# Performance work log

Measured on AMD Instinct MI355X. Metric: run time of the kernel, lower is better.

## Reference

```python
import jax, jax.numpy as jnp
import numpy as np

N_NODES = 50000
N_EDGES = 1600000
IN_NF, IN_EF, H1, H2, OUT_NF = 64, 16, 32, 32, 64
MH1, MH2, MH3 = 64, 128, 64


def _linear_params(key, fan_in, fan_out):
    kw, kb = jax.random.split(key)
    s = 1.0 / np.sqrt(fan_in)
    W = jax.random.uniform(kw, (fan_in, fan_out), minval=-s, maxval=s, dtype=jnp.float32)
    b = jax.random.uniform(kb, (fan_out,), minval=-s, maxval=s, dtype=jnp.float32)
    return W, b


def setup_inputs() -> dict:
    key = jax.random.key(0)
    ks = jax.random.split(key, 12)
    nf = jax.random.normal(ks[0], (N_NODES, IN_NF), dtype=jnp.float32)
    ef = jax.random.normal(ks[1], (N_EDGES, IN_EF), dtype=jnp.float32)
    src = jax.random.randint(ks[2], (N_EDGES,), 0, N_NODES)
    dst = jax.random.randint(ks[3], (N_EDGES,), 0, N_NODES)
    # MLP_msg: (2*in_nf+in_ef) -> 64 -> 128 -> 64 -> (1+h1+h2)
    Wm1, bm1 = _linear_params(ks[4], 2 * IN_NF + IN_EF, MH1)
    Wm2, bm2 = _linear_params(ks[5], MH1, MH2)
    Wm3, bm3 = _linear_params(ks[6], MH2, MH3)
    Wm4, bm4 = _linear_params(ks[7], MH3, 1 + H1 + H2)
    # MLP_reduce: (in_nf+h1+h2) -> 64 -> 128 -> 64 -> out_nf
    Wr1, br1 = _linear_params(ks[8], IN_NF + H1 + H2, MH1)
    Wr2, br2 = _linear_params(ks[9], MH1, MH2)
    Wr3, br3 = _linear_params(ks[10], MH2, MH3)
    Wr4, br4 = _linear_params(ks[11], MH3, OUT_NF)
    return {"nf": nf, "ef": ef, "src": src, "dst": dst,
            "Wm1": Wm1, "bm1": bm1, "Wm2": Wm2, "bm2": bm2,
            "Wm3": Wm3, "bm3": bm3, "Wm4": Wm4, "bm4": bm4,
            "Wr1": Wr1, "br1": br1, "Wr2": Wr2, "br2": br2,
            "Wr3": Wr3, "br3": br3, "Wr4": Wr4, "br4": br4}


def _mlp(x, Ws, bs):
    n = len(Ws)
    for i, (W, b) in enumerate(zip(Ws, bs)):
        x = x @ W + b
        if i < n - 1:
            x = jax.nn.leaky_relu(x, negative_slope=0.2)
    return x


def reference(nf, ef, src, dst,
              Wm1, bm1, Wm2, bm2, Wm3, bm3, Wm4, bm4,
              Wr1, br1, Wr2, br2, Wr3, br3, Wr4, br4):
    # edge_udf: gather src/dst node feats + edge feats, per-edge MLP, sigmoid gate
    x = jnp.concatenate([nf[src], nf[dst], ef], axis=1)  # [E, 2*in_nf+in_ef]
    x = _mlp(x, [Wm1, Wm2, Wm3, Wm4], [bm1, bm2, bm3, bm4])  # [E, 1+h1+h2]
    k = jax.nn.sigmoid(x[:, :1])
    ef1 = x[:, 1:1 + H1] * k
    ef2 = x[:, 1 + H1:] * k
    # update_all: scatter-sum of ef1, scatter-max of ef2 onto destination nodes
    nf1 = jax.ops.segment_sum(ef1, dst, num_segments=N_NODES)
    nf2 = jax.ops.segment_max(ef2, dst, num_segments=N_NODES)
    nf2 = jnp.where(jnp.isfinite(nf2), nf2, 0.0)  # DGL fills 0 for nodes with no in-edges
    y = jnp.concatenate([nf, nf1, nf2], axis=1)  # [N, in_nf+h1+h2]
    return _mlp(y, [Wr1, Wr2, Wr3, Wr4], [br1, br2, br3, br4])
```

## Files before the change

kernel.cpp:

```cpp
#include <hip/hip_runtime.h>

typedef unsigned int u32;
typedef __attribute__((ext_vector_type(8))) short short8;
typedef __attribute__((ext_vector_type(4))) short short4v;
typedef __attribute__((ext_vector_type(4))) float f32x4;

__device__ __forceinline__ float lrelu(float x){ return x > 0.f ? x : 0.2f*x; }

__device__ __forceinline__ void atomicMaxF(float* a, float v){
  if (__float_as_int(v) >= 0) atomicMax((int*)a, __float_as_int(v));
  else                        atomicMin((u32*)a, __float_as_uint(v));
}

__global__ void init_ws(float* __restrict__ nf1, float* __restrict__ nf2, int n32){
  int i = blockIdx.x*blockDim.x + threadIdx.x;
  int st = gridDim.x*blockDim.x;
  for (; i < n32; i += st){ nf1[i] = 0.f; nf2[i] = -__builtin_inff(); }
}

struct HL { short hi, lo; };
__device__ __forceinline__ HL split1(float x){
  u32 u = __float_as_uint(x);
  u32 r = u + 0x7FFFu + ((u >> 16) & 1u);
  float l = x - __uint_as_float(r & 0xFFFF0000u);
  HL o; o.hi = (short)(r >> 16); o.lo = (short)(__float_as_uint(l) >> 16);
  return o;
}

__device__ __forceinline__ void gatherB(const float* __restrict__ W, int K, int Nout,
                                        int kbase, int n, short8& hi, short8& lo){
  #pragma unroll
  for (int j = 0; j < 8; ++j){
    int k = kbase + j;
    float w = (k < K && n < Nout) ? W[(size_t)k * Nout + n] : 0.f;
    HL s = split1(w); hi[j] = s.hi; lo[j] = s.lo;
  }
}

__device__ __forceinline__ f32x4 mfma3(short8 ah, short8 al, short8 bh, short8 bl, f32x4 c){
  c = __builtin_amdgcn_mfma_f32_16x16x32_bf16(ah, bh, c, 0, 0, 0);
  c = __builtin_amdgcn_mfma_f32_16x16x32_bf16(al, bh, c, 0, 0, 0);
  c = __builtin_amdgcn_mfma_f32_16x16x32_bf16(ah, bl, c, 0, 0, 0);
  return c;
}

__device__ __forceinline__ void sstore1(short* hp, short* lp, int idx, float x){
  HL s = split1(x); hp[idx] = s.hi; lp[idx] = s.lo;
}
__device__ __forceinline__ void sstore4(short* hp, short* lp, int idx, f32x4 v){
  short4v h, l;
  #pragma unroll
  for (int j = 0; j < 4; ++j){ HL s = split1(v[j]); h[j] = s.hi; l[j] = s.lo; }
  *(short4v*)(hp + idx) = h;
  *(short4v*)(lp + idx) = l;
}

__global__ __launch_bounds__(256, 2) void node_pre(
    const float* __restrict__ nf, const float* __restrict__ Wm1,
    float* __restrict__ P, int N)
{
  __shared__ short Xnh[32*72];
  __shared__ short Xnl[32*72];

  const int lane = threadIdx.x & 63, wv = threadIdx.x >> 6;
  const int nl = lane & 15, quad = lane >> 4;
  const int nb = wv;
  const int slot = wv*4 + quad;

  short8 Bah[2], Bal[2], Bbh[2], Bbl[2];
  #pragma unroll
  for (int kc = 0; kc < 2; ++kc){
    gatherB(Wm1, 144, 64, kc*32 + quad*8,      nb*16 + nl, Bah[kc], Bal[kc]);
    gatherB(Wm1, 144, 64, 64 + kc*32 + quad*8, nb*16 + nl, Bbh[kc], Bbl[kc]);
  }

  const int ntiles = (N + 31) >> 5;
  for (int t = blockIdx.x; t < ntiles; t += gridDim.x){
    const int base = t << 5;
    #pragma unroll
    for (int r2 = 0; r2 < 2; ++r2){
      int row = slot*2 + r2;
      int n = base + row;
      int nc = n < N ? n : 0;
      f32x4 v = *(const f32x4*)(nf + (size_t)nc*64 + nl*4);
      sstore4(Xnh, Xnl, row*72 + nl*4, v);
    }
    __syncthreads();

    f32x4 aa[2] = {{0,0,0,0},{0,0,0,0}};
    f32x4 ab[2] = {{0,0,0,0},{0,0,0,0}};
    #pragma unroll
    for (int kc = 0; kc < 2; ++kc)
      #pragma unroll
      for (int mb = 0; mb < 2; ++mb){
        int ro = (mb*16 + nl)*72 + kc*32 + quad*8;
        short8 ah = *(const short8*)(Xnh + ro);
        short8 al = *(const short8*)(Xnl + ro);
        aa[mb] = mfma3(ah, al, Bah[kc], Bal[kc], aa[mb]);
        ab[mb] = mfma3(ah, al, Bbh[kc], Bbl[kc], ab[mb]);
      }
    #pragma unroll
    for (int mb = 0; mb < 2; ++mb)
      #pragma unroll
      for (int r = 0; r < 4; ++r){
        int n = base + mb*16 + quad*4 + r;
        if (n < N){
          P[(size_t)n*128 +      nb*16 + nl] = aa[mb][r];
          P[(size_t)n*128 + 64 + nb*16 + nl] = ab[mb][r];
        }
      }
    __syncthreads();
  }
}

#define PXES  40
#define PSS   68
#define PH1S  72
#define PH2S  136
#define POFF_XEL  1280
#define POFF_S    2560
#define POFF_H1H  6912
#define POFF_H1L  9216
#define POFF_H2H  11520
#define POFF_H2L  15872
#define POFF_DST  20224
#define P_LDS_SHORTS 20352
#define P_LDS_BYTES  (P_LDS_SHORTS*2)

__global__ __launch_bounds__(256, 2) void edge_mfma_p(
    const float* __restrict__ P, const float* __restrict__ ef,
    const int* __restrict__ src, const int* __restrict__ dst,
    const float* __restrict__ Wm1, const float* __restrict__ bm1,
    const float* __restrict__ Wm2, const float* __restrict__ bm2,
    const float* __restrict__ Wm3, const float* __restrict__ bm3,
    const float* __restrict__ Wm4, const float* __restrict__ bm4,
    float* __restrict__ nf1, float* __restrict__ nf2, int E)
{
  extern __shared__ short smem[];
  short* Xeh = smem;
  short* Xel = smem + POFF_XEL;
  float* Sb  = (float*)(smem + POFF_S);
  short* H1h = smem + POFF_H1H;
  short* H1l = smem + POFF_H1L;
  short* H2h = smem + POFF_H2H;
  short* H2l = smem + POFF_H2L;
  int*  dstI = (int*)(smem + POFF_DST);

  {
    float* z = (float*)smem;
    for (int i = threadIdx.x; i < POFF_XEL; i += blockDim.x) z[i] = 0.f;
  }

  const int lane = threadIdx.x & 63, wv = threadIdx.x >> 6;
  const int nl = lane & 15, quad = lane >> 4;
  const int nb1 = wv;
  const int slot = wv*4 + quad;

  short8 B1ch, B1cl;
  gatherB(Wm1, 144, 64, 128 + quad*8, nb1*16 + nl, B1ch, B1cl);
  short8 B2h[2][2], B2l[2][2];
  #pragma unroll
  for (int i = 0; i < 2; ++i)
    #pragma unroll
    for (int kc = 0; kc < 2; ++kc) gatherB(Wm2, 64, 128, kc*32 + quad*8, (nb1 + i*4)*16 + nl, B2h[i][kc], B2l[i][kc]);
  short8 B3h[4], B3l[4];
  #pragma unroll
  for (int kc = 0; kc < 4; ++kc) gatherB(Wm3, 128, 64,  kc*32 + quad*8, nb1*16 + nl, B3h[kc], B3l[kc]);
  short8 B4h[2], B4l[2];
  #pragma unroll
  for (int kc = 0; kc < 2; ++kc) gatherB(Wm4, 64, 65, kc*32 + quad*8, nb1*16 + nl, B4h[kc], B4l[kc]);
  const int gcol = (nl < 8) ? 0 : 64;
  short8 Bgh[2], Bgl[2];
  #pragma unroll
  for (int kc = 0; kc < 2; ++kc) gatherB(Wm4, 64, 65, kc*32 + quad*8, gcol, Bgh[kc], Bgl[kc]);

  const float bi1  = bm1[nb1*16 + nl];
  const float bi2a = bm2[nb1*16 + nl], bi2b = bm2[(nb1+4)*16 + nl];
  const float bi3  = bm3[nb1*16 + nl];
  const float bi4a = bm4[nb1*16 + nl];
  const float big  = bm4[gcol];
  __syncthreads();

  const int ntiles = (E + 31) >> 5;
  int pp = 0;
  for (int t = blockIdx.x; t < ntiles; t += gridDim.x, pp ^= 1){
    #pragma unroll
    for (int r2 = 0; r2 < 2; ++r2){
      int row = slot*2 + r2;
      int e = (t << 5) + row;
      int ec = e < E ? e : 0;
      int s = src[ec], d = dst[ec];
      f32x4 a = *(const f32x4*)(P + (size_t)s*128 +      nl*4);
      f32x4 b = *(const f32x4*)(P + (size_t)d*128 + 64 + nl*4);
      f32x4 sv = a + b;
      *(f32x4*)(Sb + row*PSS + nl*4) = sv;
      if (nl < 4){
        f32x4 v2 = *(const f32x4*)(ef + (size_t)ec*16 + nl*4);
        sstore4(Xeh, Xel, row*PXES + nl*4, v2);
      }
      if (nl == 5) dstI[pp*32 + row] = (e < E) ? d : -1;
    }
    __syncthreads();

    {
      f32x4 a1[2] = {{bi1,bi1,bi1,bi1},{bi1,bi1,bi1,bi1}};
      #pragma unroll
      for (int mb = 0; mb < 2; ++mb){
        int ro = (mb*16 + nl)*PXES + quad*8;
        short8 ah = *(const short8*)(Xeh + ro);
        short8 al = *(const short8*)(Xel + ro);
        a1[mb] = mfma3(ah, al, B1ch, B1cl, a1[mb]);
      }
      #pragma unroll
      for (int mb = 0; mb < 2; ++mb)
        #pragma unroll
        for (int r = 0; r < 4; ++r){
          int row = mb*16 + quad*4 + r;
          float sv = Sb[row*PSS + nb1*16 + nl];
          sstore1(H1h, H1l, row*PH1S + nb1*16 + nl, lrelu(a1[mb][r] + sv));
        }
    }
    __syncthreads();

    {
      f32x4 a2a[2] = {{bi2a,bi2a,bi2a,bi2a},{bi2a,bi2a,bi2a,bi2a}};
      f32x4 a2b[2] = {{bi2b,bi2b,bi2b,bi2b},{bi2b,bi2b,bi2b,bi2b}};
      #pragma unroll
      for (int kc = 0; kc < 2; ++kc)
        #pragma unroll
        for (int mb = 0; mb < 2; ++mb){
          int ro = (mb*16 + nl)*PH1S + kc*32 + quad*8;
          short8 ah = *(const short8*)(H1h + ro);
          short8 al = *(const short8*)(H1l + ro);
          a2a[mb] = mfma3(ah, al, B2h[0][kc], B2l[0][kc], a2a[mb]);
          a2b[mb] = mfma3(ah, al, B2h[1][kc], B2l[1][kc], a2b[mb]);
        }
      #pragma unroll
      for (int mb = 0; mb < 2; ++mb)
        #pragma unroll
        for (int r = 0; r < 4; ++r){
          int row = mb*16 + quad*4 + r;
          sstore1(H2h, H2l, row*PH2S + nb1*16 + nl,     lrelu(a2a[mb][r]));
          sstore1(H2h, H2l, row*PH2S + (nb1+4)*16 + nl, lrelu(a2b[mb][r]));
        }
    }
    __syncthreads();

    {
      f32x4 a3[2] = {{bi3,bi3,bi3,bi3},{bi3,bi3,bi3,bi3}};
      #pragma unroll
      for (int kc = 0; kc < 4; ++kc)
        #pragma unroll
        for (int mb = 0; mb < 2; ++mb){
          int ro = (mb*16 + nl)*PH2S + kc*32 + quad*8;
          short8 ah = *(const short8*)(H2h + ro);
          short8 al = *(const short8*)(H2l + ro);
          a3[mb] = mfma3(ah, al, B3h[kc], B3l[kc], a3[mb]);
        }
      #pragma unroll
      for (int mb = 0; mb < 2; ++mb)
        #pragma unroll
        for (int r = 0; r < 4; ++r)
          sstore1(H1h, H1l, (mb*16 + quad*4 + r)*PH1S + nb1*16 + nl, lrelu(a3[mb][r]));
    }
    __syncthreads();

    {
      f32x4 a4[2] = {{bi4a,bi4a,bi4a,bi4a},{bi4a,bi4a,bi4a,bi4a}};
      f32x4 ag[2] = {{big,big,big,big},{big,big,big,big}};
      #pragma unroll
      for (int kc = 0; kc < 2; ++kc)
        #pragma unroll
        for (int mb = 0; mb < 2; ++mb){
          int ro = (mb*16 + nl)*PH1S + kc*32 + quad*8;
          short8 ah = *(const short8*)(H1h + ro);
          short8 al = *(const short8*)(H1l + ro);
          a4[mb] = mfma3(ah, al, B4h[kc], B4l[kc], a4[mb]);
          ag[mb] = mfma3(ah, al, Bgh[kc], Bgl[kc], ag[mb]);
        }
      const int n = nb1*16 + nl;
      #pragma unroll
      for (int mb = 0; mb < 2; ++mb)
        #pragma unroll
        for (int r = 0; r < 4; ++r){
          int row = mb*16 + quad*4 + r;
          float glog = __shfl(ag[mb][r], lane & 0x30);
          float g = 1.f/(1.f + __expf(-glog));
          int d = dstI[pp*32 + row];
          if (d >= 0){
            float v = a4[mb][r] * g;
            if (n >= 1 && n <= 32)  atomicAdd(nf1 + (size_t)d*32 + (n-1), v);
            else if (n >= 33)       atomicMaxF(nf2 + (size_t)d*32 + (n-33), v);
            if (nb1 == 0 && nl == 8)
              atomicMaxF(nf2 + (size_t)d*32 + 31, ag[mb][r] * g);
          }
        }
    }
  }
}

#define XS   168
#define H1S  72
#define H2S  136
#define OFF_XL   5376
#define OFF_H2H  0
#define OFF_H2L  4352
#define OFF_H1H  10752
#define OFF_H1L  13056
#define OFF_DST  15360
#define LDS_SHORTS 15488
#define LDS_BYTES  (LDS_SHORTS*2)

__global__ __launch_bounds__(256, 2) void edge_mfma(
    const float* __restrict__ nf, const float* __restrict__ ef,
    const int* __restrict__ src, const int* __restrict__ dst,
    const float* __restrict__ Wm1, const float* __restrict__ bm1,
    const float* __restrict__ Wm2, const float* __restrict__ bm2,
    const float* __restrict__ Wm3, const float* __restrict__ bm3,
    const float* __restrict__ Wm4, const float* __restrict__ bm4,
    float* __restrict__ nf1, float* __restrict__ nf2, int E)
{
  extern __shared__ short smem[];
  short* Xh  = smem;
  short* Xl  = smem + OFF_XL;
  short* H2h = smem + OFF_H2H;
  short* H2l = smem + OFF_H2L;
  short* H1h = smem + OFF_H1H;
  short* H1l = smem + OFF_H1L;
  int*  dstI = (int*)(smem + OFF_DST);

  const int lane = threadIdx.x & 63, wv = threadIdx.x >> 6;
  const int nl = lane & 15, quad = lane >> 4;
  const int nb1 = wv;
  const int slot = wv*4 + quad;

  short8 B1h[5], B1l[5];
  #pragma unroll
  for (int kc = 0; kc < 5; ++kc) gatherB(Wm1, 144, 64,  kc*32 + quad*8, nb1*16 + nl, B1h[kc], B1l[kc]);
  short8 B2h[2][2], B2l[2][2];
  #pragma unroll
  for (int i = 0; i < 2; ++i)
    #pragma unroll
    for (int kc = 0; kc < 2; ++kc) gatherB(Wm2, 64, 128, kc*32 + quad*8, (nb1 + i*4)*16 + nl, B2h[i][kc], B2l[i][kc]);
  short8 B3h[4], B3l[4];
  #pragma unroll
  for (int kc = 0; kc < 4; ++kc) gatherB(Wm3, 128, 64,  kc*32 + quad*8, nb1*16 + nl, B3h[kc], B3l[kc]);
  short8 B4h[2], B4l[2];
  #pragma unroll
  for (int kc = 0; kc < 2; ++kc) gatherB(Wm4, 64, 65, kc*32 + quad*8, nb1*16 + nl, B4h[kc], B4l[kc]);
  const int gcol = (nl < 8) ? 0 : 64;
  short8 Bgh[2], Bgl[2];
  #pragma unroll
  for (int kc = 0; kc < 2; ++kc) gatherB(Wm4, 64, 65, kc*32 + quad*8, gcol, Bgh[kc], Bgl[kc]);

  const float bi1  = bm1[nb1*16 + nl];
  const float bi2a = bm2[nb1*16 + nl], bi2b = bm2[(nb1+4)*16 + nl];
  const float bi3  = bm3[nb1*16 + nl];
  const float bi4a = bm4[nb1*16 + nl];
  const float big  = bm4[gcol];

  const int ntiles = (E + 31) >> 5;
  int pp = 0;
  for (int t = blockIdx.x; t < ntiles; t += gridDim.x, pp ^= 1){
    #pragma unroll
    for (int r2 = 0; r2 < 2; ++r2){
      int row = slot*2 + r2;
      int e = (t << 5) + row;
      int ec = e < E ? e : 0;
      int s = src[ec], d = dst[ec];
      f32x4 v0 = *(const f32x4*)(nf + (size_t)s*64 + nl*4);
      f32x4 v1 = *(const f32x4*)(nf + (size_t)d*64 + nl*4);
      sstore4(Xh, Xl, row*XS + nl*4,      v0);
      sstore4(Xh, Xl, row*XS + 64 + nl*4, v1);
      if (nl < 4){
        f32x4 v2 = *(const f32x4*)(ef + (size_t)ec*16 + nl*4);
        sstore4(Xh, Xl, row*XS + 128 + nl*4, v2);
      } else if (nl < 8){
        short4v z = {0,0,0,0};
        *(short4v*)(Xh + row*XS + 144 + (nl-4)*4) = z;
        *(short4v*)(Xl + row*XS + 144 + (nl-4)*4) = z;
      }
      if (nl == 5) dstI[pp*32 + row] = (e < E) ? d : -1;
    }
    __syncthreads();

    {
      f32x4 a1[2] = {{bi1,bi1,bi1,bi1},{bi1,bi1,bi1,bi1}};
      #pragma unroll
      for (int kc = 0; kc < 5; ++kc)
        #pragma unroll
        for (int mb = 0; mb < 2; ++mb){
          int ro = (mb*16 + nl)*XS + kc*32 + quad*8;
          short8 ah = *(const short8*)(Xh + ro);
          short8 al = *(const short8*)(Xl + ro);
          a1[mb] = mfma3(ah, al, B1h[kc], B1l[kc], a1[mb]);
        }
      #pragma unroll
      for (int mb = 0; mb < 2; ++mb)
        #pragma unroll
        for (int r = 0; r < 4; ++r)
          sstore1(H1h, H1l, (mb*16 + quad*4 + r)*H1S + nb1*16 + nl, lrelu(a1[mb][r]));
    }
    __syncthreads();

    {
      f32x4 a2a[2] = {{bi2a,bi2a,bi2a,bi2a},{bi2a,bi2a,bi2a,bi2a}};
      f32x4 a2b[2] = {{bi2b,bi2b,bi2b,bi2b},{bi2b,bi2b,bi2b,bi2b}};
      #pragma unroll
      for (int kc = 0; kc < 2; ++kc)
        #pragma unroll
        for (int mb = 0; mb < 2; ++mb){
          int ro = (mb*16 + nl)*H1S + kc*32 + quad*8;
          short8 ah = *(const short8*)(H1h + ro);
          short8 al = *(const short8*)(H1l + ro);
          a2a[mb] = mfma3(ah, al, B2h[0][kc], B2l[0][kc], a2a[mb]);
          a2b[mb] = mfma3(ah, al, B2h[1][kc], B2l[1][kc], a2b[mb]);
        }
      #pragma unroll
      for (int mb = 0; mb < 2; ++mb)
        #pragma unroll
        for (int r = 0; r < 4; ++r){
          int row = mb*16 + quad*4 + r;
          sstore1(H2h, H2l, row*H2S + nb1*16 + nl,     lrelu(a2a[mb][r]));
          sstore1(H2h, H2l, row*H2S + (nb1+4)*16 + nl, lrelu(a2b[mb][r]));
        }
    }
    __syncthreads();

    {
      f32x4 a3[2] = {{bi3,bi3,bi3,bi3},{bi3,bi3,bi3,bi3}};
      #pragma unroll
      for (int kc = 0; kc < 4; ++kc)
        #pragma unroll
        for (int mb = 0; mb < 2; ++mb){
          int ro = (mb*16 + nl)*H2S + kc*32 + quad*8;
          short8 ah = *(const short8*)(H2h + ro);
          short8 al = *(const short8*)(H2l + ro);
          a3[mb] = mfma3(ah, al, B3h[kc], B3l[kc], a3[mb]);
        }
      #pragma unroll
      for (int mb = 0; mb < 2; ++mb)
        #pragma unroll
        for (int r = 0; r < 4; ++r)
          sstore1(H1h, H1l, (mb*16 + quad*4 + r)*H1S + nb1*16 + nl, lrelu(a3[mb][r]));
    }
    __syncthreads();

    {
      f32x4 a4[2] = {{bi4a,bi4a,bi4a,bi4a},{bi4a,bi4a,bi4a,bi4a}};
      f32x4 ag[2] = {{big,big,big,big},{big,big,big,big}};
      #pragma unroll
      for (int kc = 0; kc < 2; ++kc)
        #pragma unroll
        for (int mb = 0; mb < 2; ++mb){
          int ro = (mb*16 + nl)*H1S + kc*32 + quad*8;
          short8 ah = *(const short8*)(H1h + ro);
          short8 al = *(const short8*)(H1l + ro);
          a4[mb] = mfma3(ah, al, B4h[kc], B4l[kc], a4[mb]);
          ag[mb] = mfma3(ah, al, Bgh[kc], Bgl[kc], ag[mb]);
        }
      const int n = nb1*16 + nl;
      #pragma unroll
      for (int mb = 0; mb < 2; ++mb)
        #pragma unroll
        for (int r = 0; r < 4; ++r){
          int row = mb*16 + quad*4 + r;
          float glog = __shfl(ag[mb][r], lane & 0x30);
          float g = 1.f/(1.f + __expf(-glog));
          int d = dstI[pp*32 + row];
          if (d >= 0){
            float v = a4[mb][r] * g;
            if (n >= 1 && n <= 32)  atomicAdd(nf1 + (size_t)d*32 + (n-1), v);
            else if (n >= 33)       atomicMaxF(nf2 + (size_t)d*32 + (n-33), v);
            if (nb1 == 0 && nl == 8)
              atomicMaxF(nf2 + (size_t)d*32 + 31, ag[mb][r] * g);
          }
        }
    }
  }
}

__device__ void zero_f(float* p, int n){
  for (int i = threadIdx.x; i < n; i += blockDim.x) p[i] = 0.f;
}

#define B1S 68
#define C0S 132

__device__ __forceinline__ void splitA(const float* arow, int k0, short8& hi, short8& lo){
  f32x4 x0 = *(const f32x4*)(arow + k0);
  f32x4 x1 = *(const f32x4*)(arow + k0 + 4);
  #pragma unroll
  for (int j = 0; j < 4; ++j){
    HL a = split1(x0[j]); hi[j]   = a.hi; lo[j]   = a.lo;
    HL b = split1(x1[j]); hi[4+j] = b.hi; lo[4+j] = b.lo;
  }
}

__global__ __launch_bounds__(512, 2) void node_mfma(
    const float* __restrict__ nf,
    const float* __restrict__ nf1, const float* __restrict__ nf2,
    const float* __restrict__ Wr1, const float* __restrict__ br1,
    const float* __restrict__ Wr2, const float* __restrict__ br2,
    const float* __restrict__ Wr3, const float* __restrict__ br3,
    const float* __restrict__ Wr4, const float* __restrict__ br4,
    float* __restrict__ out, int N)
{
  __shared__ float buf0[32*C0S];
  __shared__ float buf1[32*B1S];

  zero_f(buf0, 32*C0S);
  zero_f(buf1, 32*B1S);

  const int lane = threadIdx.x & 63, wv = threadIdx.x >> 6;
  const int nl = lane & 15, quad = lane >> 4;
  const int m = wv >> 2, nb = wv & 3;

  short8 B1h[4], B1l[4];
  #pragma unroll
  for (int kc = 0; kc < 4; ++kc) gatherB(Wr1, 128, 64,  kc*32 + quad*8, nb*16 + nl, B1h[kc], B1l[kc]);
  short8 B2h[2][2], B2l[2][2];
  #pragma unroll
  for (int i = 0; i < 2; ++i)
    #pragma unroll
    for (int kc = 0; kc < 2; ++kc) gatherB(Wr2, 64, 128, kc*32 + quad*8, (nb + i*4)*16 + nl, B2h[i][kc], B2l[i][kc]);
  short8 B3h[4], B3l[4];
  #pragma unroll
  for (int kc = 0; kc < 4; ++kc) gatherB(Wr3, 128, 64,  kc*32 + quad*8, nb*16 + nl, B3h[kc], B3l[kc]);
  short8 B4h[2], B4l[2];
  #pragma unroll
  for (int kc = 0; kc < 2; ++kc) gatherB(Wr4, 64, 64,   kc*32 + quad*8, nb*16 + nl, B4h[kc], B4l[kc]);

  const float bi1  = br1[nb*16 + nl];
  const float bi2a = br2[nb*16 + nl], bi2b = br2[(nb+4)*16 + nl];
  const float bi3  = br3[nb*16 + nl];
  const float bi4  = br4[nb*16 + nl];
  __syncthreads();

  const int ntiles = (N + 31) >> 5;
  for (int t = blockIdx.x; t < ntiles; t += gridDim.x){
    const int base = t << 5;
    {
      int row = wv*4 + quad;
      int n = base + row;
      int nc = n < N ? n : 0;
      *(f32x4*)(buf0 + row*C0S + nl*4) = *(const f32x4*)(nf + (size_t)nc*64 + nl*4);
      if (nl < 8){
        *(f32x4*)(buf0 + row*C0S + 64 + nl*4) = *(const f32x4*)(nf1 + (size_t)nc*32 + nl*4);
      } else {
        f32x4 v = *(const f32x4*)(nf2 + (size_t)nc*32 + (nl-8)*4);
        #pragma unroll
        for (int j = 0; j < 4; ++j) if (!(v[j] >= -3.0e38f)) v[j] = 0.f;
        *(f32x4*)(buf0 + row*C0S + 96 + (nl-8)*4) = v;
      }
    }
    __syncthreads();

    f32x4 a1 = {bi1, bi1, bi1, bi1};
    {
      const float* arow = buf0 + (m*16 + nl)*C0S;
      #pragma unroll
      for (int kc = 0; kc < 4; ++kc){
        short8 ah, al; splitA(arow, kc*32 + quad*8, ah, al);
        a1 = mfma3(ah, al, B1h[kc], B1l[kc], a1);
      }
    }
    #pragma unroll
    for (int r = 0; r < 4; ++r)
      buf1[(m*16 + quad*4 + r)*B1S + nb*16 + nl] = lrelu(a1[r]);
    __syncthreads();

    f32x4 a2a = {bi2a, bi2a, bi2a, bi2a}, a2b = {bi2b, bi2b, bi2b, bi2b};
    {
      const float* arow = buf1 + (m*16 + nl)*B1S;
      #pragma unroll
      for (int kc = 0; kc < 2; ++kc){
        short8 ah, al; splitA(arow, kc*32 + quad*8, ah, al);
        a2a = mfma3(ah, al, B2h[0][kc], B2l[0][kc], a2a);
        a2b = mfma3(ah, al, B2h[1][kc], B2l[1][kc], a2b);
      }
    }
    #pragma unroll
    for (int r = 0; r < 4; ++r){
      buf0[(m*16 + quad*4 + r)*C0S + nb*16 + nl]     = lrelu(a2a[r]);
      buf0[(m*16 + quad*4 + r)*C0S + (nb+4)*16 + nl] = lrelu(a2b[r]);
    }
    __syncthreads();

    f32x4 a3 = {bi3, bi3, bi3, bi3};
    {
      const float* arow = buf0 + (m*16 + nl)*C0S;
      #pragma unroll
      for (int kc = 0; kc < 4; ++kc){
        short8 ah, al; splitA(arow, kc*32 + quad*8, ah, al);
        a3 = mfma3(ah, al, B3h[kc], B3l[kc], a3);
      }
    }
    #pragma unroll
    for (int r = 0; r < 4; ++r)
      buf1[(m*16 + quad*4 + r)*B1S + nb*16 + nl] = lrelu(a3[r]);
    __syncthreads();

    f32x4 a4 = {bi4, bi4, bi4, bi4};
    {
      const float* arow = buf1 + (m*16 + nl)*B1S;
      #pragma unroll
      for (int kc = 0; kc < 2; ++kc){
        short8 ah, al; splitA(arow, kc*32 + quad*8, ah, al);
        a4 = mfma3(ah, al, B4h[kc], B4l[kc], a4);
      }
    }
    #pragma unroll
    for (int r = 0; r < 4; ++r){
      int n = base + m*16 + quad*4 + r;
      if (n < N) out[(size_t)n*64 + nb*16 + nl] = a4[r];
    }
  }
}

extern "C" void kernel_launch(void* const* d_in, const int* in_sizes, int n_in,
                              void* d_out, int out_size, void* d_ws, size_t ws_size,
                              hipStream_t stream) {
  const float* nf  = (const float*)d_in[0];
  const float* ef  = (const float*)d_in[1];
  const int*   src = (const int*)d_in[2];
  const int*   dst = (const int*)d_in[3];

  const int N = in_sizes[0] / 64;
  const int E = in_sizes[2];

  float* nf1 = (float*)d_ws;
  float* nf2 = nf1 + (size_t)N * 32;
  float* P   = nf2 + (size_t)N * 32;

  size_t need = (size_t)N * 64 * 4 + (size_t)N * 128 * 4;
  bool useP = (ws_size >= need);

  static bool attr_set = false;
  if (!attr_set){
    hipFuncSetAttribute((const void*)edge_mfma,
                        hipFuncAttributeMaxDynamicSharedMemorySize, LDS_BYTES);
    hipFuncSetAttribute((const void*)edge_mfma_p,
                        hipFuncAttributeMaxDynamicSharedMemorySize, P_LDS_BYTES);
    attr_set = true;
  }

  init_ws<<<2048, 256, 0, stream>>>(nf1, nf2, N * 32);

  if (useP){
    node_pre<<<1024, 256, 0, stream>>>(nf, (const float*)d_in[4], P, N);
    edge_mfma_p<<<2048, 256, P_LDS_BYTES, stream>>>(
        P, ef, src, dst,
        (const float*)d_in[4],  (const float*)d_in[5],  (const float*)d_in[6],  (const float*)d_in[7],
        (const float*)d_in[8],  (const float*)d_in[9],  (const float*)d_in[10], (const float*)d_in[11],
        nf1, nf2, E);
  } else {
    edge_mfma<<<2048, 256, LDS_BYTES, stream>>>(
        nf, ef, src, dst,
        (const float*)d_in[4],  (const float*)d_in[5],  (const float*)d_in[6],  (const float*)d_in[7],
        (const float*)d_in[8],  (const float*)d_in[9],  (const float*)d_in[10], (const float*)d_in[11],
        nf1, nf2, E);
  }

  node_mfma<<<512, 512, 0, stream>>>(
      nf, nf1, nf2,
      (const float*)d_in[12], (const float*)d_in[13], (const float*)d_in[14], (const float*)d_in[15],
      (const float*)d_in[16], (const float*)d_in[17], (const float*)d_in[18], (const float*)d_in[19],
      (float*)d_out, N);
}
```

Baseline: 1.126 ms.

## Double-buffer edge tile staging to overlap gathers with MLP compute

Restructures the edge MLP loop so the gather of P rows, edge features and dst indices for the next tile is issued after layer 1 and runs during layers 2-4 of the current tile, using double-buffered X, S and H1 regions in LDS. Barriers become a raw lgkmcnt wait plus s_barrier, which does not wait on outstanding global loads. The aim is to hide gather latency behind MFMA work. In exchange LDS use grows from about 40KB to about 64KB per block, which may limit occupancy, and the next-tile loads hold extra registers across the compute stages.

```diff
diff --git a/kernel.cpp b/kernel.cpp
--- a/kernel.cpp
+++ b/kernel.cpp
@@ -6,6 +6,9 @@
 typedef __attribute__((ext_vector_type(4))) float f32x4;
 
 __device__ __forceinline__ float lrelu(float x){ return x > 0.f ? x : 0.2f*x; }
+
+#define BAR_LGKM() do { asm volatile("s_waitcnt lgkmcnt(0)" ::: "memory"); \
+                        __builtin_amdgcn_s_barrier(); } while(0)
 
 __device__ __forceinline__ void atomicMaxF(float* a, float v){
   if (__float_as_int(v) >= 0) atomicMax((int*)a, __float_as_int(v));
@@ -117,14 +120,15 @@
 #define PSS   68
 #define PH1S  72
 #define PH2S  136
-#define POFF_XEL  1280
-#define POFF_S    2560
-#define POFF_H1H  6912
-#define POFF_H1L  9216
-#define POFF_H2H  11520
-#define POFF_H2L  15872
-#define POFF_DST  20224
-#define P_LDS_SHORTS 20352
+#define POFF_XEH  0
+#define POFF_XEL  2560
+#define POFF_S    5120
+#define POFF_H1H  13824
+#define POFF_H1L  18432
+#define POFF_H2H  23040
+#define POFF_H2L  27392
+#define POFF_DST  31744
+#define P_LDS_SHORTS 31872
 #define P_LDS_BYTES  (P_LDS_SHORTS*2)
 
 __global__ __launch_bounds__(256, 2) void edge_mfma_p(
@@ -137,18 +141,12 @@
     float* __restrict__ nf1, float* __restrict__ nf2, int E)
 {
   extern __shared__ short smem[];
-  short* Xeh = smem;
-  short* Xel = smem + POFF_XEL;
-  float* Sb  = (float*)(smem + POFF_S);
-  short* H1h = smem + POFF_H1H;
-  short* H1l = smem + POFF_H1L;
-  short* H2h = smem + POFF_H2H;
-  short* H2l = smem + POFF_H2L;
-  int*  dstI = (int*)(smem + POFF_DST);
+  float* Sbase = (float*)(smem + POFF_S);
+  int*   dstI  = (int*)(smem + POFF_DST);
 
   {
     float* z = (float*)smem;
-    for (int i = threadIdx.x; i < POFF_XEL; i += blockDim.x) z[i] = 0.f;
+    for (int i = threadIdx.x; i < POFF_S/2; i += blockDim.x) z[i] = 0.f;
   }
 
   const int lane = threadIdx.x & 63, wv = threadIdx.x >> 6;
@@ -179,36 +177,53 @@
   const float bi3  = bm3[nb1*16 + nl];
   const float bi4a = bm4[nb1*16 + nl];
   const float big  = bm4[gcol];
+
+  const int ntiles = (E + 31) >> 5;
+  const int stride = gridDim.x;
+
+  #define STAGE(TT, Q)                                                              \
+    do {                                                                            \
+      short* xh = smem + POFF_XEH + (Q)*1280;                                       \
+      short* xl = smem + POFF_XEL + (Q)*1280;                                       \
+      float* sb = Sbase + (Q)*2176;                                                 \
+      _Pragma("unroll")                                                             \
+      for (int r2 = 0; r2 < 2; ++r2){                                               \
+        int row = slot*2 + r2;                                                      \
+        int e = ((TT) << 5) + row;                                                  \
+        int ec = e < E ? e : 0;                                                     \
+        int s = src[ec], d = dst[ec];                                               \
+        f32x4 a = *(const f32x4*)(P + (size_t)s*128 +      nl*4);                   \
+        f32x4 b = *(const f32x4*)(P + (size_t)d*128 + 64 + nl*4);                   \
+        *(f32x4*)(sb + row*PSS + nl*4) = a + b;                                     \
+        if (nl < 4){                                                                \
+          f32x4 v2 = *(const f32x4*)(ef + (size_t)ec*16 + nl*4);                    \
+          sstore4(xh, xl, row*PXES + nl*4, v2);                                     \
+        }                                                                           \
+        if (nl == 5) dstI[(Q)*32 + row] = (e < E) ? d : -1;                         \
+      }                                                                             \
+    } while(0)
+
   __syncthreads();
-
-  const int ntiles = (E + 31) >> 5;
+  if (blockIdx.x < ntiles) STAGE(blockIdx.x, 0);
+  BAR_LGKM();
+
   int pp = 0;
-  for (int t = blockIdx.x; t < ntiles; t += gridDim.x, pp ^= 1){
-    #pragma unroll
-    for (int r2 = 0; r2 < 2; ++r2){
-      int row = slot*2 + r2;
-      int e = (t << 5) + row;
-      int ec = e < E ? e : 0;
-      int s = src[ec], d = dst[ec];
-      f32x4 a = *(const f32x4*)(P + (size_t)s*128 +      nl*4);
-      f32x4 b = *(const f32x4*)(P + (size_t)d*128 + 64 + nl*4);
-      f32x4 sv = a + b;
-      *(f32x4*)(Sb + row*PSS + nl*4) = sv;
-      if (nl < 4){
-        f32x4 v2 = *(const f32x4*)(ef + (size_t)ec*16 + nl*4);
-        sstore4(Xeh, Xel, row*PXES + nl*4, v2);
-      }
-      if (nl == 5) dstI[pp*32 + row] = (e < E) ? d : -1;
-    }
-    __syncthreads();
+  for (int t = blockIdx.x; t < ntiles; t += stride, pp ^= 1){
+    short* xh  = smem + POFF_XEH + pp*1280;
+    short* xl  = smem + POFF_XEL + pp*1280;
+    float* sb  = Sbase + pp*2176;
+    short* h1h = smem + POFF_H1H + pp*2304;
+    short* h1l = smem + POFF_H1L + pp*2304;
+    short* H2h = smem + POFF_H2H;
+    short* H2l = smem + POFF_H2L;
 
     {
       f32x4 a1[2] = {{bi1,bi1,bi1,bi1},{bi1,bi1,bi1,bi1}};
       #pragma unroll
       for (int mb = 0; mb < 2; ++mb){
         int ro = (mb*16 + nl)*PXES + quad*8;
-        short8 ah = *(const short8*)(Xeh + ro);
-        short8 al = *(const short8*)(Xel + ro);
+        short8 ah = *(const short8*)(xh + ro);
+        short8 al = *(const short8*)(xl + ro);
         a1[mb] = mfma3(ah, al, B1ch, B1cl, a1[mb]);
       }
       #pragma unroll
@@ -216,11 +231,16 @@
         #pragma unroll
         for (int r = 0; r < 4; ++r){
           int row = mb*16 + quad*4 + r;
-          float sv = Sb[row*PSS + nb1*16 + nl];
-          sstore1(H1h, H1l, row*PH1S + nb1*16 + nl, lrelu(a1[mb][r] + sv));
-        }
-    }
-    __syncthreads();
+          float sv = sb[row*PSS + nb1*16 + nl];
+          sstore1(h1h, h1l, row*PH1S + nb1*16 + nl, lrelu(a1[mb][r] + sv));
+        }
+    }
+    BAR_LGKM();
+
+    {
+      int tn = t + stride;
+      if (tn < ntiles) STAGE(tn, pp^1);
+    }
 
     {
       f32x4 a2a[2] = {{bi2a,bi2a,bi2a,bi2a},{bi2a,bi2a,bi2a,bi2a}};
@@ -230,8 +250,8 @@
         #pragma unroll
         for (int mb = 0; mb < 2; ++mb){
           int ro = (mb*16 + nl)*PH1S + kc*32 + quad*8;
-          short8 ah = *(const short8*)(H1h + ro);
-          short8 al = *(const short8*)(H1l + ro);
+          short8 ah = *(const short8*)(h1h + ro);
+          short8 al = *(const short8*)(h1l + ro);
           a2a[mb] = mfma3(ah, al, B2h[0][kc], B2l[0][kc], a2a[mb]);
           a2b[mb] = mfma3(ah, al, B2h[1][kc], B2l[1][kc], a2b[mb]);
         }
@@ -244,7 +264,7 @@
           sstore1(H2h, H2l, row*PH2S + (nb1+4)*16 + nl, lrelu(a2b[mb][r]));
         }
     }
-    __syncthreads();
+    BAR_LGKM();
 
     {
       f32x4 a3[2] = {{bi3,bi3,bi3,bi3},{bi3,bi3,bi3,bi3}};
@@ -261,9 +281,9 @@
       for (int mb = 0; mb < 2; ++mb)
         #pragma unroll
         for (int r = 0; r < 4; ++r)
-          sstore1(H1h, H1l, (mb*16 + quad*4 + r)*PH1S + nb1*16 + nl, lrelu(a3[mb][r]));
-    }
-    __syncthreads();
+          sstore1(h1h, h1l, (mb*16 + quad*4 + r)*PH1S + nb1*16 + nl, lrelu(a3[mb][r]));
+    }
+    BAR_LGKM();
 
     {
       f32x4 a4[2] = {{bi4a,bi4a,bi4a,bi4a},{bi4a,bi4a,bi4a,bi4a}};
@@ -273,8 +293,8 @@
         #pragma unroll
         for (int mb = 0; mb < 2; ++mb){
           int ro = (mb*16 + nl)*PH1S + kc*32 + quad*8;
-          short8 ah = *(const short8*)(H1h + ro);
-          short8 al = *(const short8*)(H1l + ro);
+          short8 ah = *(const short8*)(h1h + ro);
+          short8 al = *(const short8*)(h1l + ro);
           a4[mb] = mfma3(ah, al, B4h[kc], B4l[kc], a4[mb]);
           ag[mb] = mfma3(ah, al, Bgh[kc], Bgl[kc], ag[mb]);
         }
@@ -297,6 +317,7 @@
         }
     }
   }
+  #undef STAGE
 }
 
 #define XS   168
```

Result: faster. 1.053 ms (-6.5%).
